# Kernel tuning notes

Hardware: AMD Instinct MI355X
Metric: run time of the kernel (lower is better)

## Reference

```python
import jax, jax.numpy as jnp
import numpy as np

B, S, D, H = 2, 2048, 2048, 16
HD = D // H  # head_dim = 128


def setup_inputs() -> dict:
    key = jax.random.key(0)
    ks = jax.random.split(key, 5)
    scale = 1.0 / np.sqrt(D)
    return {
        "x": jax.random.normal(ks[0], (B, S, D), dtype=jnp.float32),
        "wq": jax.random.normal(ks[1], (D, D), dtype=jnp.float32) * scale,
        "wk": jax.random.normal(ks[2], (D, D), dtype=jnp.float32) * scale,
        "wv": jax.random.normal(ks[3], (D, D), dtype=jnp.float32) * scale,
        "wo": jax.random.normal(ks[4], (D, D), dtype=jnp.float32) * scale,
        "bo": jnp.zeros((D,), dtype=jnp.float32),
    }


def reference(x, wq, wk, wv, wo, bo):
    b, s, _ = x.shape
    # torch Linear: y = x @ W.T ; then view(b,s,H,HD) and transpose to (b,H,s,HD)
    q = (x @ wq.T).reshape(b, s, H, HD).transpose(0, 2, 1, 3)
    k = (x @ wk.T).reshape(b, s, H, HD).transpose(0, 2, 1, 3)
    v = (x @ wv.T).reshape(b, s, H, HD).transpose(0, 2, 1, 3)
    scores = jnp.einsum("bhqd,bhkd->bhqk", q, k)
    causal = jnp.triu(jnp.ones((s, s), dtype=bool), k=1)  # True above diagonal
    scores = jnp.where(causal[None, None], -jnp.inf, scores)
    attn = jax.nn.softmax(scores / np.sqrt(HD), axis=-1)
    # dropout p=0.0 -> identity
    ctx = jnp.einsum("bhqk,bhkd->bhqd", attn, v)
    ctx = ctx.transpose(0, 2, 1, 3).reshape(b, s, D)
    return ctx @ wo.T + bo
```

## Files before the change

kernel.cpp:

```cpp
#include <hip/hip_runtime.h>
#include <math.h>

typedef __bf16 bf16_t;
typedef __bf16 bf16x8 __attribute__((ext_vector_type(8)));
typedef float f32x4 __attribute__((ext_vector_type(4)));
typedef float f32x16 __attribute__((ext_vector_type(16)));

__device__ __forceinline__ void gload_lds16(const bf16_t* g, bf16_t* l) {
    __builtin_amdgcn_global_load_lds((const __attribute__((address_space(1))) void*)g,
                                     (__attribute__((address_space(3))) void*)l, 16, 0, 0);
}

__global__ __launch_bounds__(256) void cvt_all(const float* __restrict__ x,
                                               const float* __restrict__ wq,
                                               const float* __restrict__ wk,
                                               const float* __restrict__ wv,
                                               const float* __restrict__ wo,
                                               bf16_t* __restrict__ dst) {
    int c = blockIdx.x * 256 + threadIdx.x;
    const float* src;
    size_t off;
    if (c < 1048576) { src = x; off = c; }
    else {
        int q = (c - 1048576) >> 19;
        src = (q == 0) ? wq : (q == 1) ? wk : (q == 2) ? wv : wo;
        off = (c - 1048576) & 524287;
    }
    const float4* p = (const float4*)src + off * 2;
    float4 a = p[0], b = p[1];
    union { bf16_t h[8]; uint4 u; } pk;
    pk.h[0] = (bf16_t)a.x; pk.h[1] = (bf16_t)a.y; pk.h[2] = (bf16_t)a.z; pk.h[3] = (bf16_t)a.w;
    pk.h[4] = (bf16_t)b.x; pk.h[5] = (bf16_t)b.y; pk.h[6] = (bf16_t)b.z; pk.h[7] = (bf16_t)b.w;
    ((uint4*)dst)[c] = pk.u;
}

template <int MODE, typename OutT>
__device__ __forceinline__ void gemm_core(bf16_t* __restrict__ AsB, bf16_t* __restrict__ BsB,
                                          const bf16_t* __restrict__ A,
                                          const bf16_t* __restrict__ Bm,
                                          const float* __restrict__ bias,
                                          OutT* __restrict__ C, bf16_t* __restrict__ Vt,
                                          int M, int N, int K, int bx, int by) {
    const int tid = threadIdx.x;
    const int w = tid >> 6, l = tid & 63;
    const int l16 = l & 15, lg = l >> 4;
    const int wr = w >> 1, wc = w & 1;
    const int m0 = bx * 256, n0 = by * 128;
    const int lsw = l16 & 7;

    f32x4 acc[4][4] = {};

    auto stageA = [&](int k0, int buf) {
#pragma unroll
        for (int j = 0; j < 4; ++j) {
            int c = tid + j * 512;
            int row = c >> 3;
            int kc = (c & 7) ^ (row & 7);
            gload_lds16(A + (size_t)(m0 + row) * K + k0 + kc * 8,
                        &AsB[buf * 16384 + (j * 512 + w * 64) * 8]);
        }
    };
    auto stageB = [&](int k0, int buf) {
#pragma unroll
        for (int j = 0; j < 2; ++j) {
            int c = tid + j * 512;
            int row = c >> 3;
            int kc = (c & 7) ^ (row & 7);
            gload_lds16(Bm + (size_t)(n0 + row) * K + k0 + kc * 8,
                        &BsB[buf * 8192 + (j * 512 + w * 64) * 8]);
        }
    };

    stageA(0, 0); stageB(0, 0);
    stageA(64, 1); stageB(64, 1);
    asm volatile("s_waitcnt vmcnt(6)" ::: "memory");
    __builtin_amdgcn_s_barrier();

    const int nt = K / 64;
    int cur = 0;
    for (int t = 0; t < nt; ++t) {
        int nxt = cur + 2; if (nxt >= 3) nxt -= 3;
        const bool pf = (t + 2 < nt);
        const int k2 = (t + 2) * 64;
        const bf16_t* Asc = &AsB[cur * 16384];
        const bf16_t* Bsc = &BsB[cur * 8192];

        bf16x8 bfr[4][2], af[2][2];
#pragma unroll
        for (int nf = 0; nf < 4; ++nf)
#pragma unroll
            for (int ks = 0; ks < 2; ++ks) {
                int brow = wc * 64 + nf * 16 + l16;
                bfr[nf][ks] = *(const bf16x8*)&Bsc[brow * 64 + (((ks << 2) | lg) ^ lsw) * 8];
            }
#pragma unroll
        for (int i = 0; i < 2; ++i)
#pragma unroll
            for (int ks = 0; ks < 2; ++ks) {
                int arow = wr * 64 + i * 16 + l16;
                af[i][ks] = *(const bf16x8*)&Asc[arow * 64 + (((ks << 2) | lg) ^ lsw) * 8];
            }
        if (pf) stageA(k2, nxt);
        asm volatile("s_waitcnt lgkmcnt(0)" ::: "memory");
        __builtin_amdgcn_sched_barrier(0);
        __builtin_amdgcn_s_setprio(1);
#pragma unroll
        for (int ks = 0; ks < 2; ++ks)
#pragma unroll
            for (int i = 0; i < 2; ++i)
#pragma unroll
                for (int nf = 0; nf < 4; ++nf)
                    acc[i][nf] = __builtin_amdgcn_mfma_f32_16x16x32_bf16(af[i][ks], bfr[nf][ks], acc[i][nf], 0, 0, 0);
        __builtin_amdgcn_s_setprio(0);

        bf16x8 af2[2][2];
#pragma unroll
        for (int i = 0; i < 2; ++i)
#pragma unroll
            for (int ks = 0; ks < 2; ++ks) {
                int arow = wr * 64 + (i + 2) * 16 + l16;
                af2[i][ks] = *(const bf16x8*)&Asc[arow * 64 + (((ks << 2) | lg) ^ lsw) * 8];
            }
        if (pf) stageB(k2, nxt);
        asm volatile("s_waitcnt lgkmcnt(0)" ::: "memory");
        __builtin_amdgcn_sched_barrier(0);
        __builtin_amdgcn_s_setprio(1);
#pragma unroll
        for (int ks = 0; ks < 2; ++ks)
#pragma unroll
            for (int i = 0; i < 2; ++i)
#pragma unroll
                for (int nf = 0; nf < 4; ++nf)
                    acc[i + 2][nf] = __builtin_amdgcn_mfma_f32_16x16x32_bf16(af2[i][ks], bfr[nf][ks], acc[i + 2][nf], 0, 0, 0);
        __builtin_amdgcn_s_setprio(0);

        if (pf) asm volatile("s_waitcnt vmcnt(6)" ::: "memory");
        else    asm volatile("s_waitcnt vmcnt(0)" ::: "memory");
        __builtin_amdgcn_s_barrier();
        cur = (cur + 1 == 3) ? 0 : cur + 1;
    }

    if constexpr (MODE == 2) {
#pragma unroll
        for (int mf = 0; mf < 4; ++mf)
#pragma unroll
            for (int nf = 0; nf < 4; ++nf) {
                int col = n0 + wc * 64 + nf * 16 + l16;
                int hh = col >> 7, dh = col & 127;
                int rowbase = m0 + wr * 64 + mf * 16 + lg * 4;
                int bb = rowbase >> 11, s = rowbase & 2047;
                union { bf16_t h[4]; ushort4 u4; } pk;
#pragma unroll
                for (int r = 0; r < 4; ++r) pk.h[r] = (bf16_t)acc[mf][nf][r];
                *(ushort4*)&Vt[(((size_t)(bb * 16 + hh)) * 128 + dh) * 2048 + s] = pk.u4;
            }
    } else {
#pragma unroll
        for (int mf = 0; mf < 4; ++mf)
#pragma unroll
            for (int nf = 0; nf < 4; ++nf) {
                int col = n0 + wc * 64 + nf * 16 + l16;
                float bv = (MODE == 1) ? bias[col] : 0.f;
#pragma unroll
                for (int r = 0; r < 4; ++r) {
                    int row = m0 + wr * 64 + mf * 16 + lg * 4 + r;
                    C[(size_t)row * N + col] = (OutT)(acc[mf][nf][r] + bv);
                }
            }
    }
}

__global__ __launch_bounds__(512, 2) void gemm_qkv(const bf16_t* __restrict__ A,
                                                   const bf16_t* __restrict__ W0,
                                                   const bf16_t* __restrict__ W1,
                                                   const bf16_t* __restrict__ W2,
                                                   bf16_t* __restrict__ O0, bf16_t* __restrict__ O1,
                                                   bf16_t* __restrict__ Vt, int M, int N, int K) {
    __shared__ __align__(16) bf16_t As[3 * 256 * 64];
    __shared__ __align__(16) bf16_t Bs[3 * 128 * 64];
    int flat = blockIdx.x + 16 * (blockIdx.y + 16 * blockIdx.z);
    int idx = (flat & 7) * 96 + (flat >> 3);
    int bx = idx & 15, by = (idx >> 4) & 15, bz = idx >> 8;
    if (bz == 0)      gemm_core<0, bf16_t>(As, Bs, A, W0, nullptr, O0, nullptr, M, N, K, bx, by);
    else if (bz == 1) gemm_core<0, bf16_t>(As, Bs, A, W1, nullptr, O1, nullptr, M, N, K, bx, by);
    else              gemm_core<2, bf16_t>(As, Bs, A, W2, nullptr, (bf16_t*)nullptr, Vt, M, N, K, bx, by);
}

__global__ __launch_bounds__(512, 2) void gemm_bias_f32(const bf16_t* __restrict__ A,
                                                        const bf16_t* __restrict__ Bm,
                                                        const float* __restrict__ bias,
                                                        float* __restrict__ C, int M, int N, int K) {
    __shared__ __align__(16) bf16_t As[3 * 256 * 64];
    __shared__ __align__(16) bf16_t Bs[3 * 128 * 64];
    int flat = blockIdx.x + 16 * blockIdx.y;
    int idx = (flat & 7) * 32 + (flat >> 3);
    int bx = idx & 15, by = idx >> 4;
    gemm_core<1, float>(As, Bs, A, Bm, bias, C, nullptr, M, N, K, bx, by);
}

__global__ __launch_bounds__(256, 2) void attn_fwd(const bf16_t* __restrict__ Q,
                                                   const bf16_t* __restrict__ Kk,
                                                   const bf16_t* __restrict__ Vt,
                                                   bf16_t* __restrict__ Ctx, int S, int H) {
    const int D = H * 128;
    const int bh = blockIdx.x;
    const int y = blockIdx.y;
    const int qt = (y < 8) ? (15 - y) : (y - 8);
    const int b = bh >> 4, h = bh & 15;
    const int tid = threadIdx.x;
    const int w = tid >> 6, l = tid & 63;
    const int l32 = l & 31, hi = l >> 5;
    const int q0w = qt * 128 + w * 32;
    const int qrow = q0w + l32;

    __shared__ __align__(16) bf16_t ks[2][64 * 128];
    __shared__ __align__(16) bf16_t vs[2][128 * 64];

    bf16x8 qf[8];
    {
        const bf16_t* qp = Q + (size_t)(b * S + qrow) * D + h * 128 + hi * 8;
#pragma unroll
        for (int d = 0; d < 8; ++d) qf[d] = *(const bf16x8*)(qp + d * 16);
    }

    f32x16 ctx[4] = {};
    float mrun = -INFINITY, lrun = 0.f;
    const float Cs = 0.08838834764831845f * 1.4426950408889634f;

    auto stage = [&](int k0, int buf) {
#pragma unroll
        for (int j = 0; j < 4; ++j) {
            int c = tid + j * 256;
            int r = c >> 4;
            int c16 = (c & 15) ^ (r & 7);
            gload_lds16(Kk + (size_t)(b * S + k0 + r) * D + h * 128 + c16 * 8,
                        &ks[buf][(j * 256 + w * 64) * 8]);
            int dd = c >> 3;
            int k8 = (c & 7) ^ (dd & 7);
            gload_lds16(Vt + ((size_t)bh * 128 + dd) * S + k0 + k8 * 8,
                        &vs[buf][(j * 256 + w * 64) * 8]);
        }
    };

    stage(0, 0);
    const int nkt = 2 * qt + 2;
    int cur = 0;
    for (int kt = 0; kt < nkt; ++kt) {
        __syncthreads();
        if (kt + 1 < nkt) stage((kt + 1) * 64, cur ^ 1);
        const int k0 = kt * 64;
        if (k0 <= q0w + 31) {
            f32x16 sacc[2] = {};
#pragma unroll
            for (int d = 0; d < 8; ++d) {
#pragma unroll
                for (int t2 = 0; t2 < 2; ++t2) {
                    int row = t2 * 32 + l32;
                    int c16 = (2 * d + hi) ^ (row & 7);
                    bf16x8 kf = *(const bf16x8*)&ks[cur][(row * 16 + c16) * 8];
                    sacc[t2] = __builtin_amdgcn_mfma_f32_32x32x16_bf16(kf, qf[d], sacc[t2], 0, 0, 0);
                }
            }
            const bool diag = (k0 + 63 > q0w);
#pragma unroll
            for (int t2 = 0; t2 < 2; ++t2)
#pragma unroll
                for (int c = 0; c < 16; ++c) {
                    float s = sacc[t2][c] * Cs;
                    if (diag) {
                        int key = k0 + 32 * t2 + (c & 3) + 8 * (c >> 2) + 4 * hi;
                        if (key > qrow) s = -INFINITY;
                    }
                    sacc[t2][c] = s;
                }
            float tm[16];
#pragma unroll
            for (int c = 0; c < 16; ++c) tm[c] = fmaxf(sacc[0][c], sacc[1][c]);
#pragma unroll
            for (int sft = 8; sft; sft >>= 1)
#pragma unroll
                for (int c = 0; c < 8; ++c)
                    if (c < sft) tm[c] = fmaxf(tm[c], tm[c + sft]);
            float pmax = fmaxf(tm[0], __shfl_xor(tm[0], 32));
            if (!__all(pmax <= mrun + 8.f)) {
                float mnew = fmaxf(mrun, pmax);
                float alpha = exp2f(mrun - mnew);
                lrun *= alpha;
#pragma unroll
                for (int dblk = 0; dblk < 4; ++dblk)
#pragma unroll
                    for (int c = 0; c < 16; ++c) ctx[dblk][c] *= alpha;
                mrun = mnew;
            }
#pragma unroll
            for (int t2 = 0; t2 < 2; ++t2)
#pragma unroll
                for (int c = 0; c < 16; ++c) sacc[t2][c] = exp2f(sacc[t2][c] - mrun);
            float ts[16];
#pragma unroll
            for (int c = 0; c < 16; ++c) ts[c] = sacc[0][c] + sacc[1][c];
#pragma unroll
            for (int sft = 8; sft; sft >>= 1)
#pragma unroll
                for (int c = 0; c < 8; ++c)
                    if (c < sft) ts[c] += ts[c + sft];
            lrun += ts[0] + __shfl_xor(ts[0], 32);
            bf16x8 pa[4];
#pragma unroll
            for (int ksx = 0; ksx < 4; ++ksx) {
                const int t2 = ksx >> 1, cb = (ksx & 1) * 8;
                union { bf16_t hh[4]; unsigned u[2]; } Wlo, Whi;
#pragma unroll
                for (int i = 0; i < 4; ++i) {
                    Wlo.hh[i] = (bf16_t)sacc[t2][cb + i];
                    Whi.hh[i] = (bf16_t)sacc[t2][cb + 4 + i];
                }
                unsigned s0 = hi ? Wlo.u[0] : Whi.u[0];
                unsigned s1 = hi ? Wlo.u[1] : Whi.u[1];
                unsigned r0 = __shfl_xor(s0, 32);
                unsigned r1 = __shfl_xor(s1, 32);
                union { unsigned u[4]; bf16x8 v; } F;
                if (hi == 0) { F.u[0] = Wlo.u[0]; F.u[1] = Wlo.u[1]; F.u[2] = r0; F.u[3] = r1; }
                else         { F.u[0] = r0; F.u[1] = r1; F.u[2] = Whi.u[0]; F.u[3] = Whi.u[1]; }
                pa[ksx] = F.v;
            }
#pragma unroll
            for (int ksx = 0; ksx < 4; ++ksx)
#pragma unroll
                for (int dblk = 0; dblk < 4; ++dblk) {
                    int dd = dblk * 32 + l32;
                    int k8 = (2 * ksx + hi) ^ (dd & 7);
                    bf16x8 vf = *(const bf16x8*)&vs[cur][(dd * 8 + k8) * 8];
                    ctx[dblk] = __builtin_amdgcn_mfma_f32_32x32x16_bf16(vf, pa[ksx], ctx[dblk], 0, 0, 0);
                }
        }
        cur ^= 1;
    }
    float invl = 1.f / lrun;
    bf16_t* op = Ctx + (size_t)(b * S + qrow) * D + h * 128;
#pragma unroll
    for (int dblk = 0; dblk < 4; ++dblk)
#pragma unroll
        for (int cg = 0; cg < 4; ++cg) {
            union { bf16_t hh[4]; ushort4 u4; } pk;
#pragma unroll
            for (int i = 0; i < 4; ++i) pk.hh[i] = (bf16_t)(ctx[dblk][cg * 4 + i] * invl);
            *(ushort4*)&op[dblk * 32 + cg * 8 + hi * 4] = pk.u4;
        }
}

extern "C" void kernel_launch(void* const* d_in, const int* in_sizes, int n_in,
                              void* d_out, int out_size, void* d_ws, size_t ws_size,
                              hipStream_t stream) {
    const int B = 2, S = 2048, D = 2048, H = 16;
    const int M = B * S;
    const float* x  = (const float*)d_in[0];
    const float* wq = (const float*)d_in[1];
    const float* wk = (const float*)d_in[2];
    const float* wv = (const float*)d_in[3];
    const float* wo = (const float*)d_in[4];
    const float* bo = (const float*)d_in[5];
    float* out = (float*)d_out;

    char* ws = (char*)d_ws;
    const size_t MB = 1024 * 1024;
    if (ws_size < 128 * MB) return;
    bf16_t* xb  = (bf16_t*)(ws);
    bf16_t* wqb = (bf16_t*)(ws + 16 * MB);
    bf16_t* wkb = (bf16_t*)(ws + 24 * MB);
    bf16_t* wvb = (bf16_t*)(ws + 32 * MB);
    bf16_t* wob = (bf16_t*)(ws + 40 * MB);
    bf16_t* qb  = (bf16_t*)(ws + 48 * MB);
    bf16_t* kb  = (bf16_t*)(ws + 64 * MB);
    bf16_t* vtb = (bf16_t*)(ws + 80 * MB);
    bf16_t* cxb = (bf16_t*)(ws + 96 * MB);

    cvt_all<<<12288, 256, 0, stream>>>(x, wq, wk, wv, wo, xb);
    gemm_qkv<<<dim3(16, 16, 3), 512, 0, stream>>>(xb, wqb, wkb, wvb, qb, kb, vtb, M, D, D);
    attn_fwd<<<dim3(32, 16), 256, 0, stream>>>(qb, kb, vtb, cxb, S, H);
    gemm_bias_f32<<<dim3(16, 16), 512, 0, stream>>>(cxb, wob, bo, out, M, D, D);
}
```

Baseline: 252.2 us.

## Use K=32 tiles in QKV GEMM to halve LDS and raise occupancy

Adds a QKV GEMM core that stages 32-wide K slices instead of 64, with a new XOR swizzle suited to 4 chunks per row. This halves shared memory per block (72KB to 36KB) and lets launch bounds request 4 blocks per CU instead of 2, aiming to hide latency through more resident waves. The output projection keeps the existing 64-wide core. The trade-off is twice as many loop iterations and barriers per block, with fewer MFMAs between synchronisations, and higher register pressure under the tighter launch bound.

```diff
diff --git a/kernel.cpp b/kernel.cpp
--- a/kernel.cpp
+++ b/kernel.cpp
@@ -34,13 +34,114 @@
     ((uint4*)dst)[c] = pk.u;
 }
 
-template <int MODE, typename OutT>
-__device__ __forceinline__ void gemm_core(bf16_t* __restrict__ AsB, bf16_t* __restrict__ BsB,
-                                          const bf16_t* __restrict__ A,
-                                          const bf16_t* __restrict__ Bm,
-                                          const float* __restrict__ bias,
-                                          OutT* __restrict__ C, bf16_t* __restrict__ Vt,
-                                          int M, int N, int K, int bx, int by) {
+template <int MODE>
+__device__ __forceinline__ void gemm_core32(bf16_t* __restrict__ AsB, bf16_t* __restrict__ BsB,
+                                            const bf16_t* __restrict__ A,
+                                            const bf16_t* __restrict__ Bm,
+                                            bf16_t* __restrict__ C, bf16_t* __restrict__ Vt,
+                                            int M, int N, int K, int bx, int by) {
+    const int tid = threadIdx.x;
+    const int w = tid >> 6, l = tid & 63;
+    const int l16 = l & 15, lg = l >> 4;
+    const int wr = w >> 1, wc = w & 1;
+    const int m0 = bx * 256, n0 = by * 128;
+
+    f32x4 acc[4][4] = {};
+
+    auto stageA = [&](int k0, int buf) {
+#pragma unroll
+        for (int j = 0; j < 2; ++j) {
+            int c = tid + j * 512;
+            int row = c >> 2;
+            int kc = (c & 3) ^ ((row >> 1) & 3);
+            gload_lds16(A + (size_t)(m0 + row) * K + k0 + kc * 8,
+                        &AsB[buf * 8192 + (j * 512 + w * 64) * 8]);
+        }
+    };
+    auto stageB = [&](int k0, int buf) {
+        int row = tid >> 2;
+        int kc = (tid & 3) ^ ((row >> 1) & 3);
+        gload_lds16(Bm + (size_t)(n0 + row) * K + k0 + kc * 8,
+                    &BsB[buf * 4096 + (w * 64) * 8]);
+    };
+
+    stageA(0, 0); stageB(0, 0);
+    stageA(32, 1); stageB(32, 1);
+    asm volatile("s_waitcnt vmcnt(3)" ::: "memory");
+    __builtin_amdgcn_s_barrier();
+
+    const int nt = K / 32;
+    int cur = 0;
+    for (int t = 0; t < nt; ++t) {
+        int nxt = cur + 2; if (nxt >= 3) nxt -= 3;
+        const bool pf = (t + 2 < nt);
+        const int k2 = (t + 2) * 32;
+        const bf16_t* Asc = &AsB[cur * 8192];
+        const bf16_t* Bsc = &BsB[cur * 4096];
+
+        bf16x8 af[4], bfr[4];
+#pragma unroll
+        for (int mf = 0; mf < 4; ++mf) {
+            int arow = wr * 64 + mf * 16 + l16;
+            af[mf] = *(const bf16x8*)&Asc[arow * 32 + (lg ^ ((arow >> 1) & 3)) * 8];
+        }
+#pragma unroll
+        for (int nf = 0; nf < 4; ++nf) {
+            int brow = wc * 64 + nf * 16 + l16;
+            bfr[nf] = *(const bf16x8*)&Bsc[brow * 32 + (lg ^ ((brow >> 1) & 3)) * 8];
+        }
+        if (pf) { stageA(k2, nxt); stageB(k2, nxt); }
+        asm volatile("s_waitcnt lgkmcnt(0)" ::: "memory");
+        __builtin_amdgcn_sched_barrier(0);
+        __builtin_amdgcn_s_setprio(1);
+#pragma unroll
+        for (int mf = 0; mf < 4; ++mf)
+#pragma unroll
+            for (int nf = 0; nf < 4; ++nf)
+                acc[mf][nf] = __builtin_amdgcn_mfma_f32_16x16x32_bf16(af[mf], bfr[nf], acc[mf][nf], 0, 0, 0);
+        __builtin_amdgcn_s_setprio(0);
+
+        if (pf) asm volatile("s_waitcnt vmcnt(3)" ::: "memory");
+        else    asm volatile("s_waitcnt vmcnt(0)" ::: "memory");
+        __builtin_amdgcn_s_barrier();
+        cur = (cur + 1 == 3) ? 0 : cur + 1;
+    }
+
+    if constexpr (MODE == 2) {
+#pragma unroll
+        for (int mf = 0; mf < 4; ++mf)
+#pragma unroll
+            for (int nf = 0; nf < 4; ++nf) {
+                int col = n0 + wc * 64 + nf * 16 + l16;
+                int hh = col >> 7, dh = col & 127;
+                int rowbase = m0 + wr * 64 + mf * 16 + lg * 4;
+                int bb = rowbase >> 11, s = rowbase & 2047;
+                union { bf16_t h[4]; ushort4 u4; } pk;
+#pragma unroll
+                for (int r = 0; r < 4; ++r) pk.h[r] = (bf16_t)acc[mf][nf][r];
+                *(ushort4*)&Vt[(((size_t)(bb * 16 + hh)) * 128 + dh) * 2048 + s] = pk.u4;
+            }
+    } else {
+#pragma unroll
+        for (int mf = 0; mf < 4; ++mf)
+#pragma unroll
+            for (int nf = 0; nf < 4; ++nf) {
+                int col = n0 + wc * 64 + nf * 16 + l16;
+#pragma unroll
+                for (int r = 0; r < 4; ++r) {
+                    int row = m0 + wr * 64 + mf * 16 + lg * 4 + r;
+                    C[(size_t)row * N + col] = (bf16_t)acc[mf][nf][r];
+                }
+            }
+    }
+}
+
+__device__ __forceinline__ void gemm_core64(bf16_t* __restrict__ AsB, bf16_t* __restrict__ BsB,
+                                            const bf16_t* __restrict__ A,
+                                            const bf16_t* __restrict__ Bm,
+                                            const float* __restrict__ bias,
+                                            float* __restrict__ C,
+                                            int M, int N, int K, int bx, int by) {
     const int tid = threadIdx.x;
     const int w = tid >> 6, l = tid & 63;
     const int l16 = l & 15, lg = l >> 4;
@@ -140,50 +241,34 @@
         cur = (cur + 1 == 3) ? 0 : cur + 1;
     }
 
-    if constexpr (MODE == 2) {
-#pragma unroll
-        for (int mf = 0; mf < 4; ++mf)
-#pragma unroll
-            for (int nf = 0; nf < 4; ++nf) {
-                int col = n0 + wc * 64 + nf * 16 + l16;
-                int hh = col >> 7, dh = col & 127;
-                int rowbase = m0 + wr * 64 + mf * 16 + lg * 4;
-                int bb = rowbase >> 11, s = rowbase & 2047;
-                union { bf16_t h[4]; ushort4 u4; } pk;
-#pragma unroll
-                for (int r = 0; r < 4; ++r) pk.h[r] = (bf16_t)acc[mf][nf][r];
-                *(ushort4*)&Vt[(((size_t)(bb * 16 + hh)) * 128 + dh) * 2048 + s] = pk.u4;
-            }
-    } else {
-#pragma unroll
-        for (int mf = 0; mf < 4; ++mf)
-#pragma unroll
-            for (int nf = 0; nf < 4; ++nf) {
-                int col = n0 + wc * 64 + nf * 16 + l16;
-                float bv = (MODE == 1) ? bias[col] : 0.f;
-#pragma unroll
-                for (int r = 0; r < 4; ++r) {
-                    int row = m0 + wr * 64 + mf * 16 + lg * 4 + r;
-                    C[(size_t)row * N + col] = (OutT)(acc[mf][nf][r] + bv);
-                }
-            }
-    }
-}
-
-__global__ __launch_bounds__(512, 2) void gemm_qkv(const bf16_t* __restrict__ A,
+#pragma unroll
+    for (int mf = 0; mf < 4; ++mf)
+#pragma unroll
+        for (int nf = 0; nf < 4; ++nf) {
+            int col = n0 + wc * 64 + nf * 16 + l16;
+            float bv = bias[col];
+#pragma unroll
+            for (int r = 0; r < 4; ++r) {
+                int row = m0 + wr * 64 + mf * 16 + lg * 4 + r;
+                C[(size_t)row * N + col] = acc[mf][nf][r] + bv;
+            }
+        }
+}
+
+__global__ __launch_bounds__(512, 4) void gemm_qkv(const bf16_t* __restrict__ A,
                                                    const bf16_t* __restrict__ W0,
                                                    const bf16_t* __restrict__ W1,
                                                    const bf16_t* __restrict__ W2,
                                                    bf16_t* __restrict__ O0, bf16_t* __restrict__ O1,
                                                    bf16_t* __restrict__ Vt, int M, int N, int K) {
-    __shared__ __align__(16) bf16_t As[3 * 256 * 64];
-    __shared__ __align__(16) bf16_t Bs[3 * 128 * 64];
+    __shared__ __align__(16) bf16_t As[3 * 256 * 32];
+    __shared__ __align__(16) bf16_t Bs[3 * 128 * 32];
     int flat = blockIdx.x + 16 * (blockIdx.y + 16 * blockIdx.z);
     int idx = (flat & 7) * 96 + (flat >> 3);
     int bx = idx & 15, by = (idx >> 4) & 15, bz = idx >> 8;
-    if (bz == 0)      gemm_core<0, bf16_t>(As, Bs, A, W0, nullptr, O0, nullptr, M, N, K, bx, by);
-    else if (bz == 1) gemm_core<0, bf16_t>(As, Bs, A, W1, nullptr, O1, nullptr, M, N, K, bx, by);
-    else              gemm_core<2, bf16_t>(As, Bs, A, W2, nullptr, (bf16_t*)nullptr, Vt, M, N, K, bx, by);
+    if (bz == 0)      gemm_core32<0>(As, Bs, A, W0, O0, nullptr, M, N, K, bx, by);
+    else if (bz == 1) gemm_core32<0>(As, Bs, A, W1, O1, nullptr, M, N, K, bx, by);
+    else              gemm_core32<2>(As, Bs, A, W2, nullptr, Vt, M, N, K, bx, by);
 }
 
 __global__ __launch_bounds__(512, 2) void gemm_bias_f32(const bf16_t* __restrict__ A,
@@ -195,7 +280,7 @@
     int flat = blockIdx.x + 16 * blockIdx.y;
     int idx = (flat & 7) * 32 + (flat >> 3);
     int bx = idx & 15, by = idx >> 4;
-    gemm_core<1, float>(As, Bs, A, Bm, bias, C, nullptr, M, N, K, bx, by);
+    gemm_core64(As, Bs, A, Bm, bias, C, M, N, K, bx, by);
 }
 
 __global__ __launch_bounds__(256, 2) void attn_fwd(const bf16_t* __restrict__ Q,
```

Result: no change. 253.6 us (median of 3 runs) (+0.6%).
